# Kernel tuning notes

Measured on AMD Instinct MI355X. Metric: run time of the kernel, lower is better.

Reference implementation:

```python
import jax, jax.numpy as jnp
import numpy as np

B, T, D = 4096, 64, 256   # batch, seq_dim, input_dim (== hidden_dim)
E = 128                   # encoding_dim
H = D                     # hidden_dim = input_dim in the original module


def setup_inputs() -> dict:
    key = jax.random.key(0)
    ks = jax.random.split(key, 7)
    s_enc = 1.0 / np.sqrt(D)
    s_ih = 1.0 / np.sqrt(H)  # torch LSTMCell init: U(-1/sqrt(H), 1/sqrt(H))
    return {
        "x": jax.random.normal(ks[0], (B, T, D), dtype=jnp.float32),
        "W_enc": jax.random.uniform(ks[1], (E, D), jnp.float32, -s_enc, s_enc),
        "b_enc": jax.random.uniform(ks[2], (E,), jnp.float32, -s_enc, s_enc),
        "W_ih": jax.random.uniform(ks[3], (4 * H, E), jnp.float32, -s_ih, s_ih),
        "b_ih": jax.random.uniform(ks[4], (4 * H,), jnp.float32, -s_ih, s_ih),
        "W_hh": jax.random.uniform(ks[5], (4 * H, H), jnp.float32, -s_ih, s_ih),
        "b_hh": jax.random.uniform(ks[6], (4 * H,), jnp.float32, -s_ih, s_ih),
    }


def reference(x, W_enc, b_enc, W_ih, b_ih, W_hh, b_hh):
    B_, T_, D_ = x.shape
    H_ = W_hh.shape[1]
    # Encoding layer + tanh, vectorized over all timesteps: [B,T,E]
    enc = jnp.tanh(jnp.einsum('btd,ed->bte', x, W_enc) + b_enc)
    # Precompute input contribution to LSTM gates: [B,T,4H]
    pre = jnp.einsum('bte,ge->btg', enc, W_ih) + b_ih

    def step(carry, pre_t):
        h, c = carry
        gates = pre_t + h @ W_hh.T + b_hh  # [B,4H], torch gate order i,f,g,o
        i_g, f_g, g_g, o_g = jnp.split(gates, 4, axis=-1)
        i_g = jax.nn.sigmoid(i_g)
        f_g = jax.nn.sigmoid(f_g)
        g_g = jnp.tanh(g_g)
        o_g = jax.nn.sigmoid(o_g)
        c = f_g * c + i_g * g_g
        h = o_g * jnp.tanh(c)
        return (h, c), h

    h0 = jnp.zeros((B_, H_), x.dtype)
    c0 = jnp.zeros((B_, H_), x.dtype)
    (h_n, _), hs = jax.lax.scan(step, (h0, c0), jnp.swapaxes(pre, 0, 1))
    hs = jnp.swapaxes(hs, 0, 1)  # [B,T,H]

    # Per-step prediction error vs next input; sqrt(square(.)) == abs(.)
    diff = hs[:, : T_ - 1, :] - x[:, 1:, :]        # [B,T-1,H]
    abs_diff = jnp.abs(diff)
    loss = jnp.sqrt(jnp.square(diff).sum(-1)).sum(1) / (T_ - 1)   # [B]
    loss_dim = abs_diff.sum(1) / (T_ - 1)                          # [B,H]
    loss_dim_t = jnp.concatenate(
        [abs_diff, jnp.zeros((B_, 1, H_), x.dtype)], axis=1)       # [B,T,H]
    return (h_n, loss, loss_dim, loss_dim_t)
```

## Files before the change

kernel.cpp:

```cpp
#include <hip/hip_runtime.h>

#define B_  4096
#define T_  64
#define D_  256
#define E_  128
#define H_  256

typedef __attribute__((ext_vector_type(8))) short short8;
typedef __attribute__((ext_vector_type(4))) float f32x4;
typedef __attribute__((ext_vector_type(16))) float f32x16;
typedef __attribute__((ext_vector_type(2))) unsigned int u32x2;

__device__ inline unsigned short f2bf(float f){
  unsigned u = __float_as_uint(f);
  u += 0x7FFFu + ((u >> 16) & 1u);
  return (unsigned short)(u >> 16);
}
__device__ inline float bf2f(unsigned short v){
  return __uint_as_float(((unsigned)v) << 16);
}
__device__ inline float sigm_(float x){ return __fdividef(1.f, 1.f + __expf(-x)); }
__device__ inline float tanh_(float x){
  float e = __expf(2.f * fminf(fmaxf(x, -15.f), 15.f));
  return __fdividef(e - 1.f, e + 1.f);
}
__device__ inline short8 ntload8(const unsigned short* p){
  return __builtin_nontemporal_load((const short8*)p);
}
__device__ inline f32x4 ntload4f(const float* p){
  return __builtin_nontemporal_load((const f32x4*)p);
}

__global__ __launch_bounds__(256) void init_kernel(
    const float* __restrict__ W_ih, const float* __restrict__ b_ih,
    const float* __restrict__ W_hh, const float* __restrict__ b_hh,
    unsigned short* __restrict__ Wf, float* __restrict__ biasc,
    unsigned short* __restrict__ hgF, int* __restrict__ cnt){
  const int idx  = blockIdx.x*256 + threadIdx.x;
  const int e    = idx & 7;
  const int l    = (idx >> 3) & 63;
  const int fk   = idx >> 9;
  const int ks   = fk % 24;
  const int nfs  = fk / 24;
  const int nf   = nfs & 3;
  const int s    = nfs >> 2;
  const int r    = l & 31;
  const int q    = r & 3;
  const int hl   = r >> 2;
  const int h    = s*32 + nf*8 + hl;
  const int k    = ks*16 + (l >> 5)*8 + e;
  const int g    = q*H_ + h;
  float v = (k < E_) ? W_ih[g*E_ + k] : W_hh[g*H_ + (k - E_)];
  Wf[idx] = f2bf(v);
  if (idx < 4*H_){
    int hh = idx >> 2, qq = idx & 3, gg = qq*H_ + hh;
    biasc[idx] = b_ih[gg] + b_hh[gg];
  }
  if (idx < 262144) ((unsigned long long*)hgF)[idx] = 0ull;
  if (idx < 8192) cnt[idx] = 0;
}

__global__ __launch_bounds__(256) void enc_kernel(
    const float* __restrict__ x, const float* __restrict__ W_enc,
    const float* __restrict__ b_enc, unsigned short* __restrict__ encF){
  __shared__ unsigned short As[128*64];
  __shared__ unsigned short Bs[128*64];
  __shared__ float bes[128];
  const int tid = threadIdx.x;
  const int lane = tid & 63, w = tid >> 6;
  const int l15 = lane & 15, lq = lane >> 4;
  const int m0 = blockIdx.x * 128;
  if (tid < 128) bes[tid] = b_enc[tid];

  f32x4 acc[16];
  #pragma unroll
  for (int i=0;i<16;i++) acc[i] = (f32x4)0.f;

  for (int kc = 0; kc < 4; ++kc){
    const int kb = kc*64;
    __syncthreads();
    #pragma unroll
    for (int i=0;i<4;i++){
      int u = i*256 + tid; int r = u>>3, sx = u&7;
      const float* sp = x + (size_t)(m0+r)*D_ + kb + sx*8;
      f32x4 v0 = ntload4f(sp);
      f32x4 v1 = ntload4f(sp+4);
      short8 pk;
      pk[0]=(short)f2bf(v0[0]); pk[1]=(short)f2bf(v0[1]); pk[2]=(short)f2bf(v0[2]); pk[3]=(short)f2bf(v0[3]);
      pk[4]=(short)f2bf(v1[0]); pk[5]=(short)f2bf(v1[1]); pk[6]=(short)f2bf(v1[2]); pk[7]=(short)f2bf(v1[3]);
      int off = (r*128 + sx*16) ^ ((r&7)<<4);
      *(short8*)((char*)As + off) = pk;
    }
    #pragma unroll
    for (int i=0;i<4;i++){
      int u = i*256 + tid; int r = u>>3, sx = u&7;
      const float* sp = W_enc + (size_t)r*D_ + kb + sx*8;
      f32x4 v0 = *(const f32x4*)sp;
      f32x4 v1 = *(const f32x4*)(sp+4);
      short8 pk;
      pk[0]=(short)f2bf(v0[0]); pk[1]=(short)f2bf(v0[1]); pk[2]=(short)f2bf(v0[2]); pk[3]=(short)f2bf(v0[3]);
      pk[4]=(short)f2bf(v1[0]); pk[5]=(short)f2bf(v1[1]); pk[6]=(short)f2bf(v1[2]); pk[7]=(short)f2bf(v1[3]);
      int off = (r*128 + sx*16) ^ ((r&7)<<4);
      *(short8*)((char*)Bs + off) = pk;
    }
    __syncthreads();
    #pragma unroll
    for (int kk=0;kk<2;kk++){
      short8 af[2];
      #pragma unroll
      for (int mi=0;mi<2;mi++){
        int r = 32*w + mi*16 + l15;
        int off = (r*128 + kk*64 + lq*16) ^ ((r&7)<<4);
        af[mi] = *(const short8*)((const char*)As + off);
      }
      #pragma unroll
      for (int nf=0;nf<8;nf++){
        int r = nf*16 + l15;
        int off = (r*128 + kk*64 + lq*16) ^ ((r&7)<<4);
        short8 bfr = *(const short8*)((const char*)Bs + off);
        #pragma unroll
        for (int mi=0;mi<2;mi++)
          acc[mi*8+nf] = __builtin_amdgcn_mfma_f32_16x16x32_bf16(af[mi], bfr, acc[mi*8+nf], 0,0,0);
      }
    }
  }
  #pragma unroll
  for (int mi=0;mi<2;mi++){
    #pragma unroll
    for (int nf=0;nf<8;nf++){
      int col = nf*16 + l15;
      float be = bes[col];
      #pragma unroll
      for (int j=0;j<4;j++){
        int bt = m0 + 32*w + mi*16 + lq*4 + j;
        int b = bt >> 6, tt = bt & 63;
        int gg = b >> 7, rg = (b >> 5) & 3, l31b = b & 31;
        int kw = col >> 4, l5b = (col >> 3) & 1, ee = col & 7;
        size_t byteoff = ((((size_t)tt*32 + gg)*32 + rg*8 + kw) << 10)
                       + (l31b + 32*l5b)*16 + ee*2;
        *(unsigned short*)((char*)encF + byteoff) = f2bf(tanh_(acc[mi*8+nf][j] + be));
      }
    }
  }
}

__global__ __launch_bounds__(1024) void rec_kernel(
    const unsigned short* __restrict__ encF,
    const unsigned short* __restrict__ Wf,
    const float* __restrict__ biasc,
    const float* __restrict__ x,
    unsigned short* __restrict__ hgF,
    int* __restrict__ cnt,
    unsigned short* __restrict__ psq,
    float* __restrict__ out_hn,
    float* __restrict__ out_ldim,
    float* __restrict__ out_ldt){
  extern __shared__ char smem[];
  char* wlds = smem;
  char* hbuf = smem + 98304;
  const int tid = threadIdx.x, lane = tid & 63, w = tid >> 6;
  const int l31 = lane & 31, l5 = lane >> 5;
  const int s  = blockIdx.x >> 5;
  const int g  = blockIdx.x & 31;
  const int b0 = g * 128;
  const int nf = w & 3, bg = w >> 2;

  {
    const short8* src = (const short8*)(Wf + (size_t)s*49152);
    short8* dst = (short8*)wlds;
    for (int i = tid; i < 6144; i += 1024) dst[i] = src[i];
    short8* hz = (short8*)hbuf;
    for (int i = tid; i < 4096; i += 1024) hz[i] = (short8)(short)0;
  }

  float biasr[16];
  #pragma unroll
  for (int reg=0; reg<16; ++reg){
    int q = reg & 3, hl = nf*8 + 2*(reg>>2) + l5;
    biasr[reg] = biasc[(s*32 + hl)*4 + q];
  }

  const char* abase = wlds + ((nf*24) << 10) + lane*16;
  const char* ebase = (const char*)encF + (((size_t)(g*32 + bg*8)) << 10) + lane*16;

  const int myrow = bg*32 + l31;
  const int swz   = (l31 & 7) << 4;
  const int hrd   = myrow*512 + l5*16;

  const int row2  = w*8 + (lane >> 3);
  const int swz2  = (row2 & 7) << 4;
  const int hord  = row2*512 + s*64 + (lane & 7)*8;
  const float* xr = x + (size_t)(b0+row2)*T_*D_ + s*32 + (lane&7)*4;
  float* ltr = out_ldt + (size_t)(b0+row2)*T_*H_ + s*32 + (lane&7)*4;

  const int sA = 2*(w&3), sB = sA + 1;

  float c[4] = {0.f,0.f,0.f,0.f};
  f32x4 ldim = (f32x4)0.f;

  __syncthreads();

  for (int t=0; t<T_; ++t){
    short8 ef[8];
    #pragma unroll
    for (int kw=0;kw<8;kw++)
      ef[kw] = ntload8((const unsigned short*)(ebase + ((size_t)t<<20) + (kw<<10)));
    f32x4 xv = (f32x4)0.f;
    if (t < T_-1) xv = ntload4f(xr + (size_t)(t+1)*D_);

    f32x16 a = (f32x16)0.f;
    #pragma unroll
    for (int ks=0; ks<8; ++ks){
      short8 A = *(const short8*)(abase + (ks<<10));
      a = __builtin_amdgcn_mfma_f32_32x32x16_bf16(A, ef[ks], a, 0,0,0);
    }

    if (t > 0 && lane == 0){
      if (sA != s){
        int guard = 0;
        while (__hip_atomic_load(cnt + (g*8+sA)*32, __ATOMIC_RELAXED,
                                 __HIP_MEMORY_SCOPE_AGENT) < t){
          if (++guard > (1<<20)) break;
          __builtin_amdgcn_s_sleep(1);
        }
      }
      if (sB != s){
        int guard = 0;
        while (__hip_atomic_load(cnt + (g*8+sB)*32, __ATOMIC_RELAXED,
                                 __HIP_MEMORY_SCOPE_AGENT) < t){
          if (++guard > (1<<20)) break;
          __builtin_amdgcn_s_sleep(1);
        }
      }
    }

    const size_t cbuf = ((size_t)(t&1)) << 21;
    #pragma unroll
    for (int i=0;i<4;i++){
      const int f = w*4 + i;
      const int bgf = f >> 4, ksf = f & 15;
      if ((ksf >> 1) != s){
        const unsigned long long* p = (const unsigned long long*)((const char*)hgF
            + cbuf + (((size_t)((g*4 + bgf)*16 + ksf)) << 10) + lane*16);
        unsigned long long d0 = __hip_atomic_load(p,   __ATOMIC_RELAXED, __HIP_MEMORY_SCOPE_AGENT);
        unsigned long long d1 = __hip_atomic_load(p+1, __ATOMIC_RELAXED, __HIP_MEMORY_SCOPE_AGENT);
        const int row = bgf*32 + l31;
        char* dst = hbuf + ((row*512 + ksf*32 + l5*16) ^ ((row&7)<<4));
        *(unsigned long long*)dst     = d0;
        *(unsigned long long*)(dst+8) = d1;
      }
    }
    __syncthreads();

    #pragma unroll
    for (int ks=0; ks<16; ++ks){
      short8 A  = *(const short8*)(abase + ((8+ks)<<10));
      short8 Bv = *(const short8*)(hbuf + ((hrd + ks*32) ^ swz));
      a = __builtin_amdgcn_mfma_f32_32x32x16_bf16(A, Bv, a, 0,0,0);
    }
    __syncthreads();

    #pragma unroll
    for (int r2=0; r2<4; ++r2){
      float gi = sigm_(a[r2*4+0] + biasr[r2*4+0]);
      float gf = sigm_(a[r2*4+1] + biasr[r2*4+1]);
      float gg = tanh_(a[r2*4+2] + biasr[r2*4+2]);
      float go = sigm_(a[r2*4+3] + biasr[r2*4+3]);
      float cn = gf*c[r2] + gi*gg;
      c[r2] = cn;
      float hn = go * tanh_(cn);
      int hl = nf*8 + 2*r2 + l5;
      *(unsigned short*)(hbuf + ((myrow*512 + (s*32+hl)*2) ^ swz)) = f2bf(hn);
    }
    __syncthreads();

    if (t < T_-1){
      if (w < 8){
        int bgr = w >> 1, kwl = w & 1;
        int rrow = bgr*32 + l31;
        short8 hv8 = *(const short8*)(hbuf +
            ((rrow*512 + s*64 + kwl*32 + l5*16) ^ ((rrow&7)<<4)));
        union { short8 sv; unsigned long long u[2]; } cv; cv.sv = hv8;
        unsigned long long* dstp = (unsigned long long*)((char*)hgF
            + (((size_t)((t+1)&1))<<21)
            + (((size_t)((g*4 + bgr)*16 + s*2 + kwl)) << 10) + lane*16);
        __hip_atomic_store(dstp,   cv.u[0], __ATOMIC_RELAXED, __HIP_MEMORY_SCOPE_AGENT);
        __hip_atomic_store(dstp+1, cv.u[1], __ATOMIC_RELAXED, __HIP_MEMORY_SCOPE_AGENT);
      }
      __syncthreads();
      if (tid == 0)
        __hip_atomic_fetch_add(cnt + (g*8+s)*32, 1, __ATOMIC_RELAXED,
                               __HIP_MEMORY_SCOPE_AGENT);
    }

    u32x2 hb = *(const u32x2*)(hbuf + (hord ^ swz2));
    f32x4 hf;
    hf[0] = bf2f((unsigned short)(hb[0] & 0xFFFFu));
    hf[1] = bf2f((unsigned short)(hb[0] >> 16));
    hf[2] = bf2f((unsigned short)(hb[1] & 0xFFFFu));
    hf[3] = bf2f((unsigned short)(hb[1] >> 16));
    float* ltp = ltr + (size_t)t*H_;
    if (t < T_-1){
      f32x4 d;
      d[0] = fabsf(hf[0] - xv[0]);
      d[1] = fabsf(hf[1] - xv[1]);
      d[2] = fabsf(hf[2] - xv[2]);
      d[3] = fabsf(hf[3] - xv[3]);
      __builtin_nontemporal_store(d, (f32x4*)ltp);
      ldim += d;
      float ss = d[0]*d[0] + d[1]*d[1] + d[2]*d[2] + d[3]*d[3];
      ss += __shfl_xor(ss, 1);
      ss += __shfl_xor(ss, 2);
      ss += __shfl_xor(ss, 4);
      if ((lane & 7) == 0)
        psq[((size_t)t*8 + s)*4096 + b0 + row2] = f2bf(ss);
    } else {
      __builtin_nontemporal_store((f32x4)0.f, (f32x4*)ltp);
      __builtin_nontemporal_store(hf,
          (f32x4*)(out_hn + (size_t)(b0+row2)*H_ + s*32 + (lane&7)*4));
    }
  }

  *(f32x4*)(out_ldim + (size_t)(b0+row2)*H_ + s*32 + (lane&7)*4) = ldim * (1.f/63.f);
}

__global__ __launch_bounds__(256) void final_kernel(
    const unsigned short* __restrict__ psq, float* __restrict__ out_loss){
  const int w = threadIdx.x >> 6, lane = threadIdx.x & 63;
  const int b = (blockIdx.x*4 + w)*64 + lane;
  float lacc = 0.f;
  for (int t=0;t<T_-1;++t){
    float sum = 0.f;
    #pragma unroll
    for (int s=0;s<8;s++) sum += bf2f(psq[((size_t)t*8 + s)*4096 + b]);
    lacc += sqrtf(sum);
  }
  out_loss[b] = lacc * (1.f/63.f);
}

extern "C" void kernel_launch(void* const* d_in, const int* in_sizes, int n_in,
                              void* d_out, int out_size, void* d_ws, size_t ws_size,
                              hipStream_t stream){
  const float* x     = (const float*)d_in[0];
  const float* W_enc = (const float*)d_in[1];
  const float* b_enc = (const float*)d_in[2];
  const float* W_ih  = (const float*)d_in[3];
  const float* b_ih  = (const float*)d_in[4];
  const float* W_hh  = (const float*)d_in[5];
  const float* b_hh  = (const float*)d_in[6];

  char* ws = (char*)d_ws;
  unsigned short* encF  = (unsigned short*)(ws);
  unsigned short* Wf    = (unsigned short*)(ws + 67108864);
  float*          biasc = (float*)         (ws + 67895296);
  unsigned short* hgF   = (unsigned short*)(ws + 67899392);
  int*            cnt   = (int*)           (ws + 72093696);
  unsigned short* psq   = (unsigned short*)(ws + 72126464);

  float* out_hn   = (float*)d_out;
  float* out_loss = out_hn  + (size_t)B_*H_;
  float* out_ldim = out_loss + B_;
  float* out_ldt  = out_ldim + (size_t)B_*H_;

  (void)hipFuncSetAttribute((const void*)rec_kernel,
      hipFuncAttributeMaxDynamicSharedMemorySize, 163840);

  init_kernel<<<1536, 256, 0, stream>>>(W_ih, b_ih, W_hh, b_hh, Wf, biasc, hgF, cnt);
  enc_kernel<<<2048, 256, 0, stream>>>(x, W_enc, b_enc, encF);
  rec_kernel<<<256, 1024, 163840, stream>>>(encF, Wf, biasc, x, hgF, cnt, psq,
                                            out_hn, out_ldim, out_ldt);
  final_kernel<<<16, 256, 0, stream>>>(psq, out_loss);
}
```

Baseline: 823.4 us.

## Store LDS hidden state in MFMA fragment layout and batch cross-block loads

The hidden-state LDS buffer moves from a swizzled row-major layout to the same 1 KB per-fragment layout used by the global exchange buffer. Remote fragments can then be copied with plain contiguous 16-byte stores, and the MFMA B operand is read with simple offsets. The four exchange loads are issued together as inline-asm system-coherent loads behind one waitcnt, replacing serialized 64-bit atomic loads. The final loss kernel is also split across four times more blocks, each reducing a time range through shared memory. The risk is new LDS bank conflicts on the scattered per-element h writes, plus the correctness burden of hand-written asm coherence flags.

```diff
diff --git a/kernel.cpp b/kernel.cpp
--- a/kernel.cpp
+++ b/kernel.cpp
@@ -182,16 +182,15 @@
 
   const char* abase = wlds + ((nf*24) << 10) + lane*16;
   const char* ebase = (const char*)encF + (((size_t)(g*32 + bg*8)) << 10) + lane*16;
-
-  const int myrow = bg*32 + l31;
-  const int swz   = (l31 & 7) << 4;
-  const int hrd   = myrow*512 + l5*16;
-
-  const int row2  = w*8 + (lane >> 3);
-  const int swz2  = (row2 & 7) << 4;
-  const int hord  = row2*512 + s*64 + (lane & 7)*8;
-  const float* xr = x + (size_t)(b0+row2)*T_*D_ + s*32 + (lane&7)*4;
-  float* ltr = out_ldt + (size_t)(b0+row2)*T_*H_ + s*32 + (lane&7)*4;
+  const char* hfb   = hbuf + ((bg*16) << 10) + lane*16;
+
+  const int row2 = w*8 + (lane >> 3);
+  const int bg2  = row2 >> 5;
+  const int cloc = (lane & 7)*4;
+  const int hfo  = ((bg2*16 + s*2 + (cloc>>4)) << 10)
+                 + ((row2 & 31) + ((cloc & 15) >> 3)*32)*16 + (cloc & 7)*2;
+  const float* xr = x + (size_t)(b0+row2)*T_*D_ + s*32 + cloc;
+  float* ltr = out_ldt + (size_t)(b0+row2)*T_*H_ + s*32 + cloc;
 
   const int sA = 2*(w&3), sB = sA + 1;
 
@@ -235,27 +234,33 @@
     }
 
     const size_t cbuf = ((size_t)(t&1)) << 21;
-    #pragma unroll
-    for (int i=0;i<4;i++){
-      const int f = w*4 + i;
-      const int bgf = f >> 4, ksf = f & 15;
-      if ((ksf >> 1) != s){
-        const unsigned long long* p = (const unsigned long long*)((const char*)hgF
-            + cbuf + (((size_t)((g*4 + bgf)*16 + ksf)) << 10) + lane*16);
-        unsigned long long d0 = __hip_atomic_load(p,   __ATOMIC_RELAXED, __HIP_MEMORY_SCOPE_AGENT);
-        unsigned long long d1 = __hip_atomic_load(p+1, __ATOMIC_RELAXED, __HIP_MEMORY_SCOPE_AGENT);
-        const int row = bgf*32 + l31;
-        char* dst = hbuf + ((row*512 + ksf*32 + l5*16) ^ ((row&7)<<4));
-        *(unsigned long long*)dst     = d0;
-        *(unsigned long long*)(dst+8) = d1;
-      }
+    short8 dv0, dv1, dv2, dv3;
+    {
+      const char* pb = (const char*)hgF + cbuf + (((size_t)(g*64 + w*4)) << 10) + lane*16;
+      if (((w*4+0) & 15) >> 1 != s)
+        asm volatile("global_load_dwordx4 %0, %1, off sc0 sc1" : "=&v"(dv0) : "v"(pb)        : "memory");
+      if (((w*4+1) & 15) >> 1 != s)
+        asm volatile("global_load_dwordx4 %0, %1, off sc0 sc1" : "=&v"(dv1) : "v"(pb+1024)   : "memory");
+      if (((w*4+2) & 15) >> 1 != s)
+        asm volatile("global_load_dwordx4 %0, %1, off sc0 sc1" : "=&v"(dv2) : "v"(pb+2048)   : "memory");
+      if (((w*4+3) & 15) >> 1 != s)
+        asm volatile("global_load_dwordx4 %0, %1, off sc0 sc1" : "=&v"(dv3) : "v"(pb+3072)   : "memory");
+    }
+    asm volatile("s_waitcnt vmcnt(0)" ::: "memory");
+    __builtin_amdgcn_sched_barrier(0);
+    {
+      char* db = hbuf + ((w*4) << 10) + lane*16;
+      if (((w*4+0) & 15) >> 1 != s) *(short8*)(db)        = dv0;
+      if (((w*4+1) & 15) >> 1 != s) *(short8*)(db + 1024) = dv1;
+      if (((w*4+2) & 15) >> 1 != s) *(short8*)(db + 2048) = dv2;
+      if (((w*4+3) & 15) >> 1 != s) *(short8*)(db + 3072) = dv3;
     }
     __syncthreads();
 
     #pragma unroll
     for (int ks=0; ks<16; ++ks){
       short8 A  = *(const short8*)(abase + ((8+ks)<<10));
-      short8 Bv = *(const short8*)(hbuf + ((hrd + ks*32) ^ swz));
+      short8 Bv = *(const short8*)(hfb + (ks<<10));
       a = __builtin_amdgcn_mfma_f32_32x32x16_bf16(A, Bv, a, 0,0,0);
     }
     __syncthreads();
@@ -270,20 +275,21 @@
       c[r2] = cn;
       float hn = go * tanh_(cn);
       int hl = nf*8 + 2*r2 + l5;
-      *(unsigned short*)(hbuf + ((myrow*512 + (s*32+hl)*2) ^ swz)) = f2bf(hn);
+      int fr = bg*16 + s*2 + (hl>>4);
+      int cl = hl & 15;
+      *(unsigned short*)(hbuf + (fr<<10) + (l31 + ((cl>>3)<<5))*16 + (cl&7)*2) = f2bf(hn);
     }
     __syncthreads();
 
     if (t < T_-1){
       if (w < 8){
         int bgr = w >> 1, kwl = w & 1;
-        int rrow = bgr*32 + l31;
-        short8 hv8 = *(const short8*)(hbuf +
-            ((rrow*512 + s*64 + kwl*32 + l5*16) ^ ((rrow&7)<<4)));
+        int fr = bgr*16 + s*2 + kwl;
+        short8 hv8 = *(const short8*)(hbuf + (fr<<10) + lane*16);
         union { short8 sv; unsigned long long u[2]; } cv; cv.sv = hv8;
         unsigned long long* dstp = (unsigned long long*)((char*)hgF
             + (((size_t)((t+1)&1))<<21)
-            + (((size_t)((g*4 + bgr)*16 + s*2 + kwl)) << 10) + lane*16);
+            + (((size_t)(g*64 + fr)) << 10) + lane*16);
         __hip_atomic_store(dstp,   cv.u[0], __ATOMIC_RELAXED, __HIP_MEMORY_SCOPE_AGENT);
         __hip_atomic_store(dstp+1, cv.u[1], __ATOMIC_RELAXED, __HIP_MEMORY_SCOPE_AGENT);
       }
@@ -293,7 +299,7 @@
                                __HIP_MEMORY_SCOPE_AGENT);
     }
 
-    u32x2 hb = *(const u32x2*)(hbuf + (hord ^ swz2));
+    u32x2 hb = *(const u32x2*)(hbuf + hfo);
     f32x4 hf;
     hf[0] = bf2f((unsigned short)(hb[0] & 0xFFFFu));
     hf[1] = bf2f((unsigned short)(hb[0] >> 16));
@@ -317,25 +323,33 @@
     } else {
       __builtin_nontemporal_store((f32x4)0.f, (f32x4*)ltp);
       __builtin_nontemporal_store(hf,
-          (f32x4*)(out_hn + (size_t)(b0+row2)*H_ + s*32 + (lane&7)*4));
-    }
-  }
-
-  *(f32x4*)(out_ldim + (size_t)(b0+row2)*H_ + s*32 + (lane&7)*4) = ldim * (1.f/63.f);
+          (f32x4*)(out_hn + (size_t)(b0+row2)*H_ + s*32 + cloc));
+    }
+  }
+
+  *(f32x4*)(out_ldim + (size_t)(b0+row2)*H_ + s*32 + cloc) = ldim * (1.f/63.f);
 }
 
 __global__ __launch_bounds__(256) void final_kernel(
     const unsigned short* __restrict__ psq, float* __restrict__ out_loss){
+  __shared__ float part[4][64];
   const int w = threadIdx.x >> 6, lane = threadIdx.x & 63;
-  const int b = (blockIdx.x*4 + w)*64 + lane;
+  const int b = blockIdx.x*64 + lane;
+  const int t0 = w*16;
+  const int nt = (w==3) ? 15 : 16;
   float lacc = 0.f;
-  for (int t=0;t<T_-1;++t){
+  for (int ti=0; ti<nt; ++ti){
+    int t = t0 + ti;
     float sum = 0.f;
     #pragma unroll
     for (int s=0;s<8;s++) sum += bf2f(psq[((size_t)t*8 + s)*4096 + b]);
     lacc += sqrtf(sum);
   }
-  out_loss[b] = lacc * (1.f/63.f);
+  part[w][lane] = lacc;
+  __syncthreads();
+  if (w == 0)
+    out_loss[b] = (part[0][lane]+part[1][lane]+part[2][lane]+part[3][lane])
+                  * (1.f/63.f);
 }
 
 extern "C" void kernel_launch(void* const* d_in, const int* in_sizes, int n_in,
@@ -369,5 +383,5 @@
   enc_kernel<<<2048, 256, 0, stream>>>(x, W_enc, b_enc, encF);
   rec_kernel<<<256, 1024, 163840, stream>>>(encF, Wf, biasc, x, hgF, cnt, psq,
                                             out_hn, out_ldim, out_ldt);
-  final_kernel<<<16, 256, 0, stream>>>(psq, out_loss);
-}
+  final_kernel<<<64, 256, 0, stream>>>(psq, out_loss);
+}
```

New measurement: 685.0 us. 16.8% less time.
